# Optimization experiments

Measured on AMD Instinct MI355X. Metric: run time of the kernel, lower is better.

Reference implementation:

```python
import jax, jax.numpy as jnp
import numpy as np

DIM = 5120
NUM_HEADS = 40
HEAD_DIM = DIM // NUM_HEADS
EPS = 1e-6


def rms_norm(x, g):
    # RMSNorm over last dim in fp32 for stability
    xf = x.astype(jnp.float32)
    inv = jax.lax.rsqrt(jnp.mean(xf * xf, axis=-1, keepdims=True) + EPS)
    return (xf * inv).astype(x.dtype) * g


def setup_inputs() -> dict:
    key = jax.random.key(0)
    ks = jax.random.split(key, 12)
    B, S, L = 1, 4096, 512
    inp = {
        "hidden_cond": jax.random.normal(ks[0], (B, S, DIM), jnp.float32),
        "hidden_uncond": jax.random.normal(ks[1], (B, S, DIM), jnp.float32),
        "context_cond": jax.random.normal(ks[2], (B, L, DIM), jnp.float32),
        "context_uncond": jax.random.normal(ks[3], (B, L, DIM), jnp.float32),
        # parameters (torch nn.Linear: y = x @ W.T + b)
        "Wq": jax.random.normal(ks[4], (DIM, DIM), jnp.float32) * (DIM ** -0.5),
        "bq": jnp.zeros((DIM,), jnp.float32),
        "Wkv": jax.random.normal(ks[5], (2 * DIM, DIM), jnp.float32) * (DIM ** -0.5),
        "bkv": jnp.zeros((2 * DIM,), jnp.float32),
        "gq": jnp.ones((DIM,), jnp.float32),
        "gk": jnp.ones((DIM,), jnp.float32),
        "Wo": jax.random.normal(ks[6], (DIM, DIM), jnp.float32) * (DIM ** -0.5),
        "bo": jnp.zeros((DIM,), jnp.float32),
    }
    return inp


def reference(hidden_cond, hidden_uncond, context_cond, context_uncond,
              Wq, bq, Wkv, bkv, gq, gk, Wo, bo):
    H, Dh = NUM_HEADS, HEAD_DIM
    scale = Dh ** -0.5

    hidden = jnp.concatenate([hidden_cond, hidden_uncond], axis=0)   # [2B, S, D]
    context = jnp.concatenate([context_cond, context_uncond], axis=0)  # [2B, L, D]
    CB, S, D = hidden.shape
    L = context.shape[1]

    q = hidden @ Wq.T + bq                    # [2B, S, D]
    q = rms_norm(q, gq)
    q = q.reshape(CB, S, H, Dh).transpose(0, 2, 1, 3)  # [2B, H, S, Dh]

    kv = context @ Wkv.T + bkv                # [2B, L, 2D]
    kv = kv.reshape(CB, L, 2, H, Dh).transpose(2, 0, 3, 1, 4)  # [2,2B,H,L,Dh]
    k, v = kv[0], kv[1]

    k_flat = k.transpose(0, 2, 1, 3).reshape(CB, L, D)
    k_flat = rms_norm(k_flat, gk)
    k = k_flat.reshape(CB, L, H, Dh).transpose(0, 2, 1, 3)  # [2B, H, L, Dh]

    attn = jnp.einsum('bhsd,bhld->bhsl', q, k) * scale
    attn = jax.nn.softmax(attn.astype(jnp.float32), axis=-1).astype(q.dtype)
    out = jnp.einsum('bhsl,bhld->bhsd', attn, v)            # [2B, H, S, Dh]
    out = out.transpose(0, 2, 1, 3).reshape(CB, S, D)
    out = out @ Wo.T + bo

    out_cond, out_uncond = jnp.split(out, 2, axis=0)
    return (out_cond, out_uncond)
```

## Files before the change

### kernel.cpp

```cpp
#include <hip/hip_runtime.h>
#include <hip/hip_bf16.h>
#include <cstdint>
#include <cstddef>

#define DIM 5120
#define NH 40
#define HD 128
#define S_LEN 4096
#define L_LEN 512
#define CBATCH 2
#define MQ (CBATCH*S_LEN)
#define ML (CBATCH*L_LEN)

typedef unsigned short ushort_t;
typedef __bf16 bf16x8 __attribute__((ext_vector_type(8)));
typedef float f32x4 __attribute__((ext_vector_type(4)));
typedef float f32x16 __attribute__((ext_vector_type(16)));

__device__ __forceinline__ ushort_t f2bf(float f) {
  union { float f; unsigned u; } c; c.f = f;
  unsigned r = c.u + 0x7fffu + ((c.u >> 16) & 1u);
  return (ushort_t)(r >> 16);
}

__device__ __forceinline__ void load_lds16(const void* g, void* l) {
  __builtin_amdgcn_global_load_lds(
      (const __attribute__((address_space(1))) void*)g,
      (__attribute__((address_space(3))) void*)l, 16, 0, 0);
}

__global__ __launch_bounds__(256) void cvt_f32_bf16(const float* __restrict__ in,
                                                    ushort_t* __restrict__ out, int n4) {
  int i = blockIdx.x * 256 + threadIdx.x;
  if (i >= n4) return;
  float4 v = *(const float4*)(in + 4ull * (size_t)i);
  ushort4 o;
  o.x = f2bf(v.x); o.y = f2bf(v.y); o.z = f2bf(v.z); o.w = f2bf(v.w);
  *(ushort4*)(out + 4ull * (size_t)i) = o;
}

template <int OUT_F32>
__global__ __launch_bounds__(512, 2) void gemm_bt8(const ushort_t* __restrict__ A,
                                                   const ushort_t* __restrict__ W,
                                                   const float* __restrict__ bias,
                                                   void* __restrict__ Cout,
                                                   int M, int N, int K) {
  __shared__ ushort_t lds[65536];
  char* ldsc = (char*)lds;
  const int tid = threadIdx.x;
  const int lane = tid & 63, w = tid >> 6;
  const int g = lane >> 4, c = lane & 15;
  const int wm = w >> 2, wn = w & 3;
  const int ntn = N >> 8;
  const int nwg = gridDim.x;
  int bid = blockIdx.x;
  bid = (bid & 7) * (nwg >> 3) + (bid >> 3);
  const int tm = bid / ntn, tn = bid % ntn;
  const size_t m0 = (size_t)tm * 256, n0 = (size_t)tn * 256;
  const ushort_t* Ab = A + m0 * (size_t)K;
  const ushort_t* Bb = W + n0 * (size_t)K;
  const int NT = K >> 6;

  const int srow = tid >> 2;
  const int sgq  = (tid & 3) ^ (((tid >> 5) & 1) << 1);
  const size_t rb0 = (size_t)srow * K + (size_t)sgq * 8;
  const size_t rb1 = rb0 + (size_t)128 * K;
  const int d0 = tid * 16;

  int offA[8], offB[4];
#pragma unroll
  for (int m = 0; m < 8; ++m) {
    int row = wm * 128 + m * 16 + c;
    offA[m] = row * 64 + ((g * 16) ^ ((row & 8) << 2));
  }
#pragma unroll
  for (int n = 0; n < 4; ++n) {
    int row = wn * 64 + n * 16 + c;
    offB[n] = row * 64 + ((g * 16) ^ ((row & 8) << 2));
  }

  auto STAGE = [&](int h) {
    const int th = h >> 2, j = h & 3;
    const int kofs = th * 64 + ((j >> 1) << 5);
    const ushort_t* gsrc = ((j & 1) ? Ab : Bb) + kofs;
    const int dbase = ((th & 1) << 16) + (j << 14);
    load_lds16(gsrc + rb0, ldsc + dbase + d0);
    load_lds16(gsrc + rb1, ldsc + dbase + 8192 + d0);
  };

  f32x4 acc[8][4] = {};

#pragma unroll
  for (int h = 0; h < 7; ++h) STAGE(h);
  asm volatile("s_waitcnt vmcnt(6)" ::: "memory");
  __builtin_amdgcn_s_barrier();

  for (int t = 0; t < NT; ++t) {
    const int buf = (t & 1) << 2;
    bf16x8 a[4], a2[4], b[4];
#pragma unroll
    for (int m = 0; m < 4; ++m)
      a[m] = *(const bf16x8*)(ldsc + ((buf + 1) << 14) + offA[m]);
#pragma unroll
    for (int n = 0; n < 4; ++n)
      b[n] = *(const bf16x8*)(ldsc + ((buf + 0) << 14) + offB[n]);
    if (t < NT - 2) STAGE(4 * t + 7);
    else if (t == NT - 2) STAGE(4 * NT - 1);
    __builtin_amdgcn_s_barrier();
    asm volatile("s_waitcnt lgkmcnt(0)" ::: "memory");
    __builtin_amdgcn_sched_barrier(0);
    __builtin_amdgcn_s_setprio(1);
#pragma unroll
    for (int m = 0; m < 4; ++m)
#pragma unroll
      for (int n = 0; n < 4; ++n)
        acc[m][n] = __builtin_amdgcn_mfma_f32_16x16x32_bf16(a[m], b[n], acc[m][n], 0, 0, 0);
    __builtin_amdgcn_s_setprio(0);
    __builtin_amdgcn_s_barrier();
#pragma unroll
    for (int m = 0; m < 4; ++m)
      a2[m] = *(const bf16x8*)(ldsc + ((buf + 1) << 14) + offA[4 + m]);
    if (t < NT - 2) STAGE(4 * t + 8);
    __builtin_amdgcn_s_barrier();
    asm volatile("s_waitcnt lgkmcnt(0)" ::: "memory");
    __builtin_amdgcn_sched_barrier(0);
    __builtin_amdgcn_s_setprio(1);
#pragma unroll
    for (int m = 0; m < 4; ++m)
#pragma unroll
      for (int n = 0; n < 4; ++n)
        acc[4 + m][n] = __builtin_amdgcn_mfma_f32_16x16x32_bf16(a2[m], b[n], acc[4 + m][n], 0, 0, 0);
    __builtin_amdgcn_s_setprio(0);
    __builtin_amdgcn_s_barrier();
#pragma unroll
    for (int m = 0; m < 4; ++m)
      a[m] = *(const bf16x8*)(ldsc + ((buf + 3) << 14) + offA[m]);
#pragma unroll
    for (int n = 0; n < 4; ++n)
      b[n] = *(const bf16x8*)(ldsc + ((buf + 2) << 14) + offB[n]);
    if (t < NT - 2) STAGE(4 * t + 9);
    __builtin_amdgcn_s_barrier();
    asm volatile("s_waitcnt lgkmcnt(0)" ::: "memory");
    __builtin_amdgcn_sched_barrier(0);
    __builtin_amdgcn_s_setprio(1);
#pragma unroll
    for (int m = 0; m < 4; ++m)
#pragma unroll
      for (int n = 0; n < 4; ++n)
        acc[m][n] = __builtin_amdgcn_mfma_f32_16x16x32_bf16(a[m], b[n], acc[m][n], 0, 0, 0);
    __builtin_amdgcn_s_setprio(0);
    __builtin_amdgcn_s_barrier();
#pragma unroll
    for (int m = 0; m < 4; ++m)
      a2[m] = *(const bf16x8*)(ldsc + ((buf + 3) << 14) + offA[4 + m]);
    if (t < NT - 2) STAGE(4 * t + 10);
    __builtin_amdgcn_s_barrier();
    asm volatile("s_waitcnt lgkmcnt(0)" ::: "memory");
    __builtin_amdgcn_sched_barrier(0);
    __builtin_amdgcn_s_setprio(1);
#pragma unroll
    for (int m = 0; m < 4; ++m)
#pragma unroll
      for (int n = 0; n < 4; ++n)
        acc[4 + m][n] = __builtin_amdgcn_mfma_f32_16x16x32_bf16(a2[m], b[n], acc[4 + m][n], 0, 0, 0);
    __builtin_amdgcn_s_setprio(0);
    if (t < NT - 2)      asm volatile("s_waitcnt vmcnt(6)" ::: "memory");
    else if (t == NT - 2) asm volatile("s_waitcnt vmcnt(0)" ::: "memory");
    __builtin_amdgcn_s_barrier();
  }

#pragma unroll
  for (int m = 0; m < 8; ++m) {
#pragma unroll
    for (int n = 0; n < 4; ++n) {
      size_t gm = m0 + wm * 128 + m * 16 + g * 4;
      size_t gn = n0 + wn * 64 + n * 16 + c;
      float bn = bias[gn];
#pragma unroll
      for (int r = 0; r < 4; ++r) {
        float v = acc[m][n][r] + bn;
        if (OUT_F32) ((float*)Cout)[(gm + r) * (size_t)N + gn] = v;
        else         ((ushort_t*)Cout)[(gm + r) * (size_t)N + gn] = f2bf(v);
      }
    }
  }
  (void)M;
}

template <int OUT_F32>
__global__ __launch_bounds__(256) void gemm_bt(const ushort_t* __restrict__ A,
                                               const ushort_t* __restrict__ W,
                                               const float* __restrict__ bias,
                                               void* __restrict__ Cout,
                                               int M, int N, int K) {
  __shared__ ushort_t sA[128 * 32];
  __shared__ ushort_t sB[128 * 32];
  const int tid = threadIdx.x;
  const int w = tid >> 6, lane = tid & 63;
  const int g = lane >> 4, c = lane & 15;
  const int ntn = N >> 7;
  const int nwg = gridDim.x;
  int bid = blockIdx.x;
  bid = (bid & 7) * (nwg >> 3) + (bid >> 3);
  const int tm = bid / ntn, tn = bid % ntn;
  const size_t m0 = (size_t)tm * 128, n0 = (size_t)tn * 128;
  const int wr = (w >> 1) * 64, wc = (w & 1) * 64;

  f32x4 acc[4][4] = {};

  const ushort_t* Abase = A + m0 * (size_t)K;
  const ushort_t* Bbase = W + n0 * (size_t)K;

  for (int k0 = 0; k0 < K; k0 += 32) {
    __syncthreads();
#pragma unroll
    for (int i = 0; i < 2; ++i) {
      int gid = i * 256 + tid;
      int row = gid >> 2, colE = (gid & 3) << 3;
      load_lds16(Abase + (size_t)row * K + k0 + colE, sA + i * 2048 + w * 512);
      load_lds16(Bbase + (size_t)row * K + k0 + colE, sB + i * 2048 + w * 512);
    }
    __syncthreads();
    bf16x8 a[4], b[4];
#pragma unroll
    for (int m = 0; m < 4; ++m)
      a[m] = *(const bf16x8*)(sA + (wr + m * 16 + c) * 32 + g * 8);
#pragma unroll
    for (int n = 0; n < 4; ++n)
      b[n] = *(const bf16x8*)(sB + (wc + n * 16 + c) * 32 + g * 8);
#pragma unroll
    for (int m = 0; m < 4; ++m)
#pragma unroll
      for (int n = 0; n < 4; ++n)
        acc[m][n] = __builtin_amdgcn_mfma_f32_16x16x32_bf16(a[m], b[n], acc[m][n], 0, 0, 0);
  }

#pragma unroll
  for (int m = 0; m < 4; ++m) {
#pragma unroll
    for (int n = 0; n < 4; ++n) {
      size_t gm = m0 + wr + m * 16 + g * 4;
      size_t gn = n0 + wc + n * 16 + c;
      float bn = bias[gn];
#pragma unroll
      for (int r = 0; r < 4; ++r) {
        float v = acc[m][n][r] + bn;
        if (OUT_F32) ((float*)Cout)[(gm + r) * (size_t)N + gn] = v;
        else         ((ushort_t*)Cout)[(gm + r) * (size_t)N + gn] = f2bf(v);
      }
    }
  }
}

__global__ __launch_bounds__(256) void rmsnorm_rows(ushort_t* __restrict__ x,
                                                    const float* __restrict__ gw,
                                                    int ncols, int stride, float oscale) {
  const int row = blockIdx.x;
  ushort_t* p = x + (size_t)row * stride;
  const int tid = threadIdx.x;
  const int nch = ncols >> 3;
  float ss = 0.f;
  for (int ci = tid; ci < nch; ci += 256) {
    bf16x8 v = *(const bf16x8*)(p + ci * 8);
#pragma unroll
    for (int j = 0; j < 8; ++j) { float f = (float)v[j]; ss += f * f; }
  }
#pragma unroll
  for (int off = 1; off < 64; off <<= 1) ss += __shfl_xor(ss, off);
  __shared__ float sred[4];
  if ((tid & 63) == 0) sred[tid >> 6] = ss;
  __syncthreads();
  float tot = sred[0] + sred[1] + sred[2] + sred[3];
  float inv = rsqrtf(tot / (float)ncols + 1e-6f) * oscale;
  for (int ci = tid; ci < nch; ci += 256) {
    bf16x8 v = *(const bf16x8*)(p + ci * 8);
    bf16x8 ov;
#pragma unroll
    for (int j = 0; j < 8; ++j) {
      float f = (float)v[j];
      ushort_t ob = f2bf(f * inv * gw[ci * 8 + j]);
      ov[j] = *(__bf16*)&ob;
    }
    *(bf16x8*)(p + ci * 8) = ov;
  }
}

__global__ __launch_bounds__(256) void transpose_v(const ushort_t* __restrict__ kv,
                                                   ushort_t* __restrict__ vt) {
  const int bh = blockIdx.y, b = bh / NH, h = bh % NH;
  const int l0 = blockIdx.x * 32;
  const ushort_t* src = kv + (size_t)b * L_LEN * (2 * DIM) + DIM + (size_t)h * HD;
  ushort_t* dst = vt + (size_t)bh * HD * L_LEN;
  __shared__ ushort_t tile[32][HD + 16];
  const int tid = threadIdx.x;
#pragma unroll
  for (int i = 0; i < 2; ++i) {
    int gid = i * 256 + tid;
    int r = gid >> 4, ce = (gid & 15) << 3;
    *(bf16x8*)(&tile[r][ce]) = *(const bf16x8*)(src + (size_t)(l0 + r) * (2 * DIM) + ce);
  }
  __syncthreads();
#pragma unroll
  for (int i = 0; i < 2; ++i) {
    int gid = i * 256 + tid;
    int d = gid >> 2, le = (gid & 3) << 3;
    bf16x8 v;
#pragma unroll
    for (int j = 0; j < 8; ++j) v[j] = *(__bf16*)&tile[le + j][d];
    *(bf16x8*)(dst + (size_t)d * L_LEN + l0 + le) = v;
  }
}

__global__ __launch_bounds__(256) void attn_fwd(const ushort_t* __restrict__ q,
                                                const ushort_t* __restrict__ kv,
                                                const ushort_t* __restrict__ vt,
                                                ushort_t* __restrict__ out) {
  const int bh = blockIdx.y, b = bh / NH, h = bh % NH;
  const int tid = threadIdx.x, w = tid >> 6, lane = tid & 63;
  const int lq = lane & 31, hi = lane >> 5;
  const int qr0 = blockIdx.x * 128 + w * 32;

  const ushort_t* qrow  = q  + ((size_t)b * S_LEN + qr0 + lq) * DIM + (size_t)h * HD + hi * 8;
  const ushort_t* krow  = kv + (size_t)b * L_LEN * (2 * DIM) + (size_t)h * HD
                             + (size_t)lq * (2 * DIM) + hi * 8;
  const ushort_t* vrow  = vt + (size_t)bh * HD * L_LEN + (size_t)lq * L_LEN + hi * 8;

  bf16x8 qf[8];
#pragma unroll
  for (int ks = 0; ks < 8; ++ks) qf[ks] = *(const bf16x8*)(qrow + ks * 16);

  f32x16 o[4];
#pragma unroll
  for (int ch = 0; ch < 4; ++ch) o[ch] = 0.f;
  float m = -1e30f, lsum = 0.f;

  for (int l0 = 0; l0 < L_LEN; l0 += 32) {
    f32x16 sv = 0.f;
#pragma unroll
    for (int ks = 0; ks < 8; ++ks) {
      bf16x8 kf = *(const bf16x8*)(krow + (size_t)l0 * (2 * DIM) + ks * 16);
      sv = __builtin_amdgcn_mfma_f32_32x32x16_bf16(kf, qf[ks], sv, 0, 0, 0);
    }
    float pm = fmaxf(fmaxf(fmaxf(sv[0], sv[1]), fmaxf(sv[2], sv[3])),
                     fmaxf(fmaxf(sv[4], sv[5]), fmaxf(sv[6], sv[7])));
    pm = fmaxf(pm, fmaxf(fmaxf(fmaxf(sv[8], sv[9]), fmaxf(sv[10], sv[11])),
                         fmaxf(fmaxf(sv[12], sv[13]), fmaxf(sv[14], sv[15]))));
    pm = fmaxf(pm, __shfl_xor(pm, 32));
    if (__ballot(pm > m + 8.0f)) {
      float mn = fmaxf(m, pm);
      float al = __builtin_amdgcn_exp2f(m - mn);
      lsum *= al;
      m = mn;
#pragma unroll
      for (int r = 0; r < 16; ++r) {
        float ar = __shfl(al, (r & 3) + 8 * (r >> 2) + 4 * hi);
        o[0][r] *= ar; o[1][r] *= ar; o[2][r] *= ar; o[3][r] *= ar;
      }
    }
    float p[16]; float ls = 0.f;
#pragma unroll
    for (int r = 0; r < 16; ++r) { p[r] = __builtin_amdgcn_exp2f(sv[r] - m); ls += p[r]; }
    ls += __shfl_xor(ls, 32);
    lsum += ls;
    bf16x8 pa[2];
#pragma unroll
    for (int ks = 0; ks < 2; ++ks) {
      unsigned w0 = (unsigned)f2bf(p[8 * ks + 0]) | ((unsigned)f2bf(p[8 * ks + 1]) << 16);
      unsigned w1 = (unsigned)f2bf(p[8 * ks + 2]) | ((unsigned)f2bf(p[8 * ks + 3]) << 16);
      unsigned w2 = (unsigned)f2bf(p[8 * ks + 4]) | ((unsigned)f2bf(p[8 * ks + 5]) << 16);
      unsigned w3 = (unsigned)f2bf(p[8 * ks + 6]) | ((unsigned)f2bf(p[8 * ks + 7]) << 16);
      unsigned e0 = __shfl_xor((int)w0, 32), e1 = __shfl_xor((int)w1, 32);
      unsigned e2 = __shfl_xor((int)w2, 32), e3 = __shfl_xor((int)w3, 32);
      unsigned d0 = hi ? e2 : w0, d1 = hi ? e3 : w1;
      unsigned d2 = hi ? w2 : e0, d3 = hi ? w3 : e1;
      unsigned tmp[4] = {d0, d1, d2, d3};
      pa[ks] = *(const bf16x8*)tmp;
    }
#pragma unroll
    for (int ch = 0; ch < 4; ++ch) {
#pragma unroll
      for (int ks = 0; ks < 2; ++ks) {
        bf16x8 vf = *(const bf16x8*)(vrow + (size_t)ch * 32 * L_LEN + l0 + ks * 16);
        o[ch] = __builtin_amdgcn_mfma_f32_32x32x16_bf16(pa[ks], vf, o[ch], 0, 0, 0);
      }
    }
  }

  float inv[16];
#pragma unroll
  for (int r = 0; r < 16; ++r) {
    float lr = __shfl(lsum, (r & 3) + 8 * (r >> 2) + 4 * hi);
    inv[r] = 1.0f / lr;
  }
  ushort_t* ob = out + ((size_t)b * S_LEN + qr0) * DIM + (size_t)h * HD;
#pragma unroll
  for (int ch = 0; ch < 4; ++ch)
#pragma unroll
    for (int r = 0; r < 16; ++r) {
      int row = (r & 3) + 8 * (r >> 2) + 4 * hi;
      ob[(size_t)row * DIM + ch * 32 + lq] = f2bf(o[ch][r] * inv[r]);
    }
}

extern "C" void kernel_launch(void* const* d_in, const int* in_sizes, int n_in,
                              void* d_out, int out_size, void* d_ws, size_t ws_size,
                              hipStream_t stream) {
  (void)in_sizes; (void)n_in; (void)out_size; (void)ws_size;
  const float* hidden_c = (const float*)d_in[0];
  const float* hidden_u = (const float*)d_in[1];
  const float* ctx_c    = (const float*)d_in[2];
  const float* ctx_u    = (const float*)d_in[3];
  const float* Wq  = (const float*)d_in[4];
  const float* bq  = (const float*)d_in[5];
  const float* Wkv = (const float*)d_in[6];
  const float* bkv = (const float*)d_in[7];
  const float* gq  = (const float*)d_in[8];
  const float* gk  = (const float*)d_in[9];
  const float* Wo  = (const float*)d_in[10];
  const float* bo  = (const float*)d_in[11];

  char* ws = (char*)d_ws;
  size_t off = 0;
  auto alloc = [&](size_t bytes) {
    char* p = ws + off; off += (bytes + 255) & ~(size_t)255; return p;
  };
  ushort_t* hbf  = (ushort_t*)alloc((size_t)MQ * DIM * 2);
  ushort_t* cbf  = (ushort_t*)alloc((size_t)ML * DIM * 2);
  ushort_t* wqb  = (ushort_t*)alloc((size_t)DIM * DIM * 2);
  ushort_t* wkvb = (ushort_t*)alloc((size_t)2 * DIM * DIM * 2);
  ushort_t* kvb  = (ushort_t*)alloc((size_t)ML * 2 * DIM * 2);
  ushort_t* vtb  = (ushort_t*)alloc((size_t)CBATCH * NH * HD * L_LEN * 2);
  ushort_t* qb   = (ushort_t*)d_out;

  auto cvt = [&](const float* in, ushort_t* o, size_t n) {
    int n4 = (int)(n >> 2);
    cvt_f32_bf16<<<dim3((n4 + 255) / 256), dim3(256), 0, stream>>>(in, o, n4);
  };
  cvt(hidden_c, hbf, (size_t)S_LEN * DIM);
  cvt(hidden_u, hbf + (size_t)S_LEN * DIM, (size_t)S_LEN * DIM);
  cvt(ctx_c, cbf, (size_t)L_LEN * DIM);
  cvt(ctx_u, cbf + (size_t)L_LEN * DIM, (size_t)L_LEN * DIM);
  cvt(Wq, wqb, (size_t)DIM * DIM);
  cvt(Wkv, wkvb, (size_t)2 * DIM * DIM);

  gemm_bt8<0><<<dim3((MQ / 256) * (DIM / 256)), dim3(512), 0, stream>>>(
      hbf, wqb, bq, (void*)qb, MQ, DIM, DIM);
  gemm_bt<0><<<dim3((ML / 128) * ((2 * DIM) / 128)), dim3(256), 0, stream>>>(
      cbf, wkvb, bkv, (void*)kvb, ML, 2 * DIM, DIM);
  cvt(Wo, wqb, (size_t)DIM * DIM);

  const float qscale = 0.08838834764831845f * 1.4426950408889634f;
  rmsnorm_rows<<<dim3(MQ), dim3(256), 0, stream>>>(qb, gq, DIM, DIM, qscale);
  rmsnorm_rows<<<dim3(ML), dim3(256), 0, stream>>>(kvb, gk, DIM, 2 * DIM, 1.0f);
  transpose_v<<<dim3(L_LEN / 32, CBATCH * NH), dim3(256), 0, stream>>>(kvb, vtb);

  attn_fwd<<<dim3(S_LEN / 128, CBATCH * NH), dim3(256), 0, stream>>>(qb, kvb, vtb, hbf);

  gemm_bt8<1><<<dim3((MQ / 256) * (DIM / 256)), dim3(512), 0, stream>>>(
      hbf, wqb, bo, d_out, MQ, DIM, DIM);
}
```

Before: 1.581 ms.

## Shrink main GEMM tile to 256x128 with triple-buffered LDS pipeline

The 8-wave bf16 GEMM used for the Q and output projections now computes 256x128 tiles instead of 256x256. The waves are arranged 4x2 and each owns a 64x64 sub-tile. The K loop becomes a three-slot LDS ring buffer that keeps two future K-tiles in flight, and the launch grid is doubled to match. This aims to improve wave quantization across the CUs (1280 tiles instead of 640) and deepen load prefetching, at the cost of lower per-tile data reuse and a larger LDS footprint (144 KB, which allows only one block per CU).

```diff
diff --git a/kernel.cpp b/kernel.cpp
--- a/kernel.cpp
+++ b/kernel.cpp
@@ -45,33 +45,33 @@
                                                    const float* __restrict__ bias,
                                                    void* __restrict__ Cout,
                                                    int M, int N, int K) {
-  __shared__ ushort_t lds[65536];
+  __shared__ ushort_t lds[73728];
   char* ldsc = (char*)lds;
   const int tid = threadIdx.x;
   const int lane = tid & 63, w = tid >> 6;
   const int g = lane >> 4, c = lane & 15;
-  const int wm = w >> 2, wn = w & 3;
-  const int ntn = N >> 8;
+  const int wm = w >> 1, wn = w & 1;
+  const int ntn = N >> 7;
   const int nwg = gridDim.x;
   int bid = blockIdx.x;
   bid = (bid & 7) * (nwg >> 3) + (bid >> 3);
   const int tm = bid / ntn, tn = bid % ntn;
-  const size_t m0 = (size_t)tm * 256, n0 = (size_t)tn * 256;
+  const size_t m0 = (size_t)tm * 256, n0 = (size_t)tn * 128;
   const ushort_t* Ab = A + m0 * (size_t)K;
   const ushort_t* Bb = W + n0 * (size_t)K;
   const int NT = K >> 6;
 
   const int srow = tid >> 2;
   const int sgq  = (tid & 3) ^ (((tid >> 5) & 1) << 1);
-  const size_t rb0 = (size_t)srow * K + (size_t)sgq * 8;
-  const size_t rb1 = rb0 + (size_t)128 * K;
+  const size_t sRB = (size_t)srow * K + (size_t)sgq * 8;
+  const size_t sRA1 = sRB + (size_t)128 * K;
   const int d0 = tid * 16;
 
-  int offA[8], offB[4];
-#pragma unroll
-  for (int m = 0; m < 8; ++m) {
-    int row = wm * 128 + m * 16 + c;
-    offA[m] = row * 64 + ((g * 16) ^ ((row & 8) << 2));
+  int offA[4], offB[4];
+#pragma unroll
+  for (int m = 0; m < 4; ++m) {
+    int row = wm * 64 + m * 16 + c;
+    offA[m] = 8192 + row * 64 + ((g * 16) ^ ((row & 8) << 2));
   }
 #pragma unroll
   for (int n = 0; n < 4; ++n) {
@@ -79,33 +79,29 @@
     offB[n] = row * 64 + ((g * 16) ^ ((row & 8) << 2));
   }
 
-  auto STAGE = [&](int h) {
-    const int th = h >> 2, j = h & 3;
-    const int kofs = th * 64 + ((j >> 1) << 5);
-    const ushort_t* gsrc = ((j & 1) ? Ab : Bb) + kofs;
-    const int dbase = ((th & 1) << 16) + (j << 14);
-    load_lds16(gsrc + rb0, ldsc + dbase + d0);
-    load_lds16(gsrc + rb1, ldsc + dbase + 8192 + d0);
+  auto STAGE = [&](int tileIdx, int slab, int bufbase) {
+    const size_t kof = (size_t)tileIdx * 64 + (size_t)(slab << 5);
+    char* db = ldsc + bufbase + slab * 24576;
+    load_lds16(Bb + sRB + kof,  db + d0);
+    load_lds16(Ab + sRB + kof,  db + 8192 + d0);
+    load_lds16(Ab + sRA1 + kof, db + 16384 + d0);
   };
 
-  f32x4 acc[8][4] = {};
-
-#pragma unroll
-  for (int h = 0; h < 7; ++h) STAGE(h);
+  f32x4 acc[4][4] = {};
+
+  STAGE(0, 0, 0); STAGE(0, 1, 0);
+  STAGE(1, 0, 49152); STAGE(1, 1, 49152);
   asm volatile("s_waitcnt vmcnt(6)" ::: "memory");
   __builtin_amdgcn_s_barrier();
 
+  int rb = 0, sb = 2 * 49152;
   for (int t = 0; t < NT; ++t) {
-    const int buf = (t & 1) << 2;
-    bf16x8 a[4], a2[4], b[4];
-#pragma unroll
-    for (int m = 0; m < 4; ++m)
-      a[m] = *(const bf16x8*)(ldsc + ((buf + 1) << 14) + offA[m]);
-#pragma unroll
-    for (int n = 0; n < 4; ++n)
-      b[n] = *(const bf16x8*)(ldsc + ((buf + 0) << 14) + offB[n]);
-    if (t < NT - 2) STAGE(4 * t + 7);
-    else if (t == NT - 2) STAGE(4 * NT - 1);
+    bf16x8 a[4], b[4];
+#pragma unroll
+    for (int m = 0; m < 4; ++m) a[m] = *(const bf16x8*)(ldsc + rb + offA[m]);
+#pragma unroll
+    for (int n = 0; n < 4; ++n) b[n] = *(const bf16x8*)(ldsc + rb + offB[n]);
+    if (t < NT - 2) STAGE(t + 2, 0, sb);
     __builtin_amdgcn_s_barrier();
     asm volatile("s_waitcnt lgkmcnt(0)" ::: "memory");
     __builtin_amdgcn_sched_barrier(0);
@@ -118,9 +114,10 @@
     __builtin_amdgcn_s_setprio(0);
     __builtin_amdgcn_s_barrier();
 #pragma unroll
-    for (int m = 0; m < 4; ++m)
-      a2[m] = *(const bf16x8*)(ldsc + ((buf + 1) << 14) + offA[4 + m]);
-    if (t < NT - 2) STAGE(4 * t + 8);
+    for (int m = 0; m < 4; ++m) a[m] = *(const bf16x8*)(ldsc + rb + 24576 + offA[m]);
+#pragma unroll
+    for (int n = 0; n < 4; ++n) b[n] = *(const bf16x8*)(ldsc + rb + 24576 + offB[n]);
+    if (t < NT - 2) STAGE(t + 2, 1, sb);
     __builtin_amdgcn_s_barrier();
     asm volatile("s_waitcnt lgkmcnt(0)" ::: "memory");
     __builtin_amdgcn_sched_barrier(0);
@@ -129,51 +126,20 @@
     for (int m = 0; m < 4; ++m)
 #pragma unroll
       for (int n = 0; n < 4; ++n)
-        acc[4 + m][n] = __builtin_amdgcn_mfma_f32_16x16x32_bf16(a2[m], b[n], acc[4 + m][n], 0, 0, 0);
-    __builtin_amdgcn_s_setprio(0);
-    __builtin_amdgcn_s_barrier();
-#pragma unroll
-    for (int m = 0; m < 4; ++m)
-      a[m] = *(const bf16x8*)(ldsc + ((buf + 3) << 14) + offA[m]);
-#pragma unroll
-    for (int n = 0; n < 4; ++n)
-      b[n] = *(const bf16x8*)(ldsc + ((buf + 2) << 14) + offB[n]);
-    if (t < NT - 2) STAGE(4 * t + 9);
-    __builtin_amdgcn_s_barrier();
-    asm volatile("s_waitcnt lgkmcnt(0)" ::: "memory");
-    __builtin_amdgcn_sched_barrier(0);
-    __builtin_amdgcn_s_setprio(1);
-#pragma unroll
-    for (int m = 0; m < 4; ++m)
-#pragma unroll
-      for (int n = 0; n < 4; ++n)
         acc[m][n] = __builtin_amdgcn_mfma_f32_16x16x32_bf16(a[m], b[n], acc[m][n], 0, 0, 0);
     __builtin_amdgcn_s_setprio(0);
-    __builtin_amdgcn_s_barrier();
-#pragma unroll
-    for (int m = 0; m < 4; ++m)
-      a2[m] = *(const bf16x8*)(ldsc + ((buf + 3) << 14) + offA[4 + m]);
-    if (t < NT - 2) STAGE(4 * t + 10);
-    __builtin_amdgcn_s_barrier();
-    asm volatile("s_waitcnt lgkmcnt(0)" ::: "memory");
-    __builtin_amdgcn_sched_barrier(0);
-    __builtin_amdgcn_s_setprio(1);
-#pragma unroll
-    for (int m = 0; m < 4; ++m)
-#pragma unroll
-      for (int n = 0; n < 4; ++n)
-        acc[4 + m][n] = __builtin_amdgcn_mfma_f32_16x16x32_bf16(a2[m], b[n], acc[4 + m][n], 0, 0, 0);
-    __builtin_amdgcn_s_setprio(0);
-    if (t < NT - 2)      asm volatile("s_waitcnt vmcnt(6)" ::: "memory");
+    if (t < NT - 2)       asm volatile("s_waitcnt vmcnt(6)" ::: "memory");
     else if (t == NT - 2) asm volatile("s_waitcnt vmcnt(0)" ::: "memory");
     __builtin_amdgcn_s_barrier();
-  }
-
-#pragma unroll
-  for (int m = 0; m < 8; ++m) {
+    rb += 49152; if (rb == 147456) rb = 0;
+    sb += 49152; if (sb == 147456) sb = 0;
+  }
+
+#pragma unroll
+  for (int m = 0; m < 4; ++m) {
 #pragma unroll
     for (int n = 0; n < 4; ++n) {
-      size_t gm = m0 + wm * 128 + m * 16 + g * 4;
+      size_t gm = m0 + wm * 64 + m * 16 + g * 4;
       size_t gn = n0 + wn * 64 + n * 16 + c;
       float bn = bias[gn];
 #pragma unroll
@@ -443,7 +409,7 @@
   cvt(Wq, wqb, (size_t)DIM * DIM);
   cvt(Wkv, wkvb, (size_t)2 * DIM * DIM);
 
-  gemm_bt8<0><<<dim3((MQ / 256) * (DIM / 256)), dim3(512), 0, stream>>>(
+  gemm_bt8<0><<<dim3((MQ / 256) * (DIM / 128)), dim3(512), 0, stream>>>(
       hbf, wqb, bq, (void*)qb, MQ, DIM, DIM);
   gemm_bt<0><<<dim3((ML / 128) * ((2 * DIM) / 128)), dim3(256), 0, stream>>>(
       cbf, wkvb, bkv, (void*)kvb, ML, 2 * DIM, DIM);
@@ -456,6 +422,6 @@
 
   attn_fwd<<<dim3(S_LEN / 128, CBATCH * NH), dim3(256), 0, stream>>>(qb, kvb, vtb, hbf);
 
-  gemm_bt8<1><<<dim3((MQ / 256) * (DIM / 256)), dim3(512), 0, stream>>>(
+  gemm_bt8<1><<<dim3((MQ / 256) * (DIM / 128)), dim3(512), 0, stream>>>(
       hbf, wqb, bo, d_out, MQ, DIM, DIM);
 }
```

New measurement: 1.718 ms. +8.6%, slower.
